# Optimization experiments

Hardware: AMD Instinct MI355X
Metric: run time of the kernel (lower is better)

The kernel has to match this reference:

```python
import jax, jax.numpy as jnp
import numpy as np

NB, B, T, D, H = 7, 16, 512, 128, 2
HD = D // H

def _ln(x, s, b):
    m = jnp.mean(x, -1, keepdims=True)
    v = jnp.mean((x - m) ** 2, -1, keepdims=True)
    return (x - m) * jax.lax.rsqrt(v + 1e-5) * s + b

def setup_inputs():
    key = jax.random.key(0)
    keys = iter(jax.random.split(key, 80))
    def w(*shape):
        return jax.random.normal(next(keys), shape, jnp.float32) * 0.02
    inp = {}
    inp['bands'] = jax.random.normal(next(keys), (NB, B, T, D), jnp.float32)
    for nm in ['Wq', 'Wk', 'Wv', 'Wo']:
        inp[nm] = w(NB, D, D)
    for nm in ['bq', 'bk', 'bv', 'bo']:
        inp[nm] = jnp.zeros((NB, D), jnp.float32)
    inp['g_ls'] = jnp.ones((3, D), jnp.float32); inp['g_lb'] = jnp.zeros((3, D), jnp.float32)
    inp['g_w1'] = w(3, D, 2 * D); inp['g_b1'] = jnp.zeros((3, 2 * D), jnp.float32)
    inp['g_w2'] = w(3, 2 * D, D); inp['g_b2'] = jnp.zeros((3, D), jnp.float32)
    inp['g_wg'] = w(3, D, D);     inp['g_bg'] = jnp.zeros((3, D), jnp.float32)
    inp['h_ls'] = jnp.ones((2, D), jnp.float32); inp['h_lb'] = jnp.zeros((2, D), jnp.float32)
    inp['h_w1'] = w(2, D, 3 * D); inp['h_b1'] = jnp.zeros((2, 3 * D), jnp.float32)
    inp['h_w2'] = w(2, 3 * D, D); inp['h_b2'] = jnp.zeros((2, D), jnp.float32)
    inp['r_ls'] = jnp.ones((2, D), jnp.float32); inp['r_lb'] = jnp.zeros((2, D), jnp.float32)
    inp['r_w1'] = w(2, D, 4 * D); inp['r_b1'] = jnp.zeros((2, 4 * D), jnp.float32)
    inp['r_w2'] = w(2, 4 * D, D); inp['r_b2'] = jnp.zeros((2, D), jnp.float32)
    # wormhole: pairs (0,6),(1,5),(2,4) share cross_proj per pair; bridge on band 3
    inp['wp_w'] = w(3, D, D);     inp['wp_b'] = jnp.zeros((3, D), jnp.float32)
    inp['wg_w'] = w(3, 2 * D, D); inp['wg_b'] = jnp.zeros((3, D), jnp.float32)
    inp['br_w'] = w(6, D, D);     inp['br_b'] = jnp.zeros((6, D), jnp.float32)
    inp['bg_w'] = w(2 * D, D);    inp['bg_b'] = jnp.zeros((D,), jnp.float32)
    return inp

def reference(bands, Wq, bq, Wk, bk, Wv, bv, Wo, bo,
              g_ls, g_lb, g_w1, g_b1, g_w2, g_b2, g_wg, g_bg,
              h_ls, h_lb, h_w1, h_b1, h_w2, h_b2,
              r_ls, r_lb, r_w1, r_b1, r_w2, r_b2,
              wp_w, wp_b, wg_w, wg_b, br_w, br_b, bg_w, bg_b):
    n, b, t, d = bands.shape
    # --- per-band causal self-attention, vectorized over the 7 bands ---
    def heads(x):  # [n,b,t,d] -> [n,b,H,t,hd]
        return x.reshape(n, b, t, H, HD).transpose(0, 1, 3, 2, 4)
    q = heads(jnp.einsum('nbtd,nde->nbte', bands, Wq) + bq[:, None, None, :])
    k = heads(jnp.einsum('nbtd,nde->nbte', bands, Wk) + bk[:, None, None, :])
    v = heads(jnp.einsum('nbtd,nde->nbte', bands, Wv) + bv[:, None, None, :])
    scores = jnp.einsum('nbhtd,nbhsd->nbhts', q, k) / np.float32(np.sqrt(HD))
    causal = jnp.triu(jnp.ones((t, t), bool), 1)
    scores = jnp.where(causal, jnp.float32(-1e9), scores)
    attn = jax.nn.softmax(scores, axis=-1)
    o = jnp.einsum('nbhts,nbhsd->nbhtd', attn, v)
    o = o.transpose(0, 1, 3, 2, 4).reshape(n, b, t, d)
    o = jnp.einsum('nbtd,nde->nbte', o, Wo) + bo[:, None, None, :]
    x = bands + o
    # --- band-tier FFN processors ---
    geo, hyb, rea = x[0:3], x[3:5], x[5:7]
    hg = _ln(geo, g_ls[:, None, None, :], g_lb[:, None, None, :])
    hg = jax.nn.gelu(jnp.einsum('nbtd,nde->nbte', hg, g_w1) + g_b1[:, None, None, :], approximate=False)
    hg = jnp.einsum('nbte,ned->nbtd', hg, g_w2) + g_b2[:, None, None, :]
    gate = jax.nn.sigmoid(jnp.einsum('nbtd,nde->nbte', geo, g_wg) + g_bg[:, None, None, :])
    geo = geo + gate * hg
    hh = _ln(hyb, h_ls[:, None, None, :], h_lb[:, None, None, :])
    hh = jax.nn.gelu(jnp.einsum('nbtd,nde->nbte', hh, h_w1) + h_b1[:, None, None, :], approximate=False)
    hyb = hyb + jnp.einsum('nbte,ned->nbtd', hh, h_w2) + h_b2[:, None, None, :]
    hr = _ln(rea, r_ls[:, None, None, :], r_lb[:, None, None, :])
    hr = jax.nn.gelu(jnp.einsum('nbtd,nde->nbte', hr, r_w1) + r_b1[:, None, None, :], approximate=False)
    rea = rea + jnp.einsum('nbte,ned->nbtd', hr, r_w2) + r_b2[:, None, None, :]
    y = jnp.concatenate([geo, hyb, rea], axis=0)
    # --- position-wise wormhole: pairs (0,6),(1,5),(2,4) + bridge band 3 ---
    bl = y[jnp.array([0, 1, 2])]   # low bands of each pair
    bh = y[jnp.array([6, 5, 4])]   # matching high bands
    info_lo = jnp.einsum('nbtd,nde->nbte', bh, wp_w) + wp_b[:, None, None, :]
    info_hi = jnp.einsum('nbtd,nde->nbte', bl, wp_w) + wp_b[:, None, None, :]
    gate_lo = jax.nn.sigmoid(jnp.einsum('nbtd,nde->nbte', jnp.concatenate([bl, info_lo], -1), wg_w) + wg_b[:, None, None, :])
    gate_hi = jax.nn.sigmoid(jnp.einsum('nbtd,nde->nbte', jnp.concatenate([bh, info_hi], -1), wg_w) + wg_b[:, None, None, :])
    out_lo = bl + gate_lo * info_lo
    out_hi = bh + gate_hi * info_hi
    others = y[jnp.array([0, 1, 2, 4, 5, 6])]
    bridge_info = (jnp.einsum('nbtd,nde->bte', others, br_w) + jnp.sum(br_b, 0)) / 6.0
    gate_br = jax.nn.sigmoid(jnp.concatenate([y[3], bridge_info], -1) @ bg_w + bg_b)
    out3 = y[3] + gate_br * bridge_info
    return jnp.stack([out_lo[0], out_lo[1], out_lo[2], out3, out_hi[2], out_hi[1], out_hi[0]], axis=0)
```

## Files before the change

### kernel.cpp

```cpp
#include <hip/hip_runtime.h>
#include <hip/hip_bf16.h>

#define NBAND 7
#define BBATCH 16
#define TSEQ 512
#define DMODEL 128
#define MBAND (BBATCH * TSEQ)
#define BANDE ((size_t)MBAND * DMODEL)

typedef __attribute__((ext_vector_type(8))) short short8;
typedef __attribute__((ext_vector_type(4))) float f32x4;
typedef unsigned int u32;
typedef unsigned short u16;

__device__ __forceinline__ u16 f2bf(float x) {
  unsigned u = __float_as_uint(x);
  unsigned r = u + 0x7FFF + ((u >> 16) & 1);
  return (u16)(r >> 16);
}
__device__ __forceinline__ u32 pack2(float a, float b) {
  return (u32)f2bf(a) | ((u32)f2bf(b) << 16);
}
__device__ __forceinline__ float b2f(u16 h) {
  return __uint_as_float((u32)h << 16);
}

struct TSlice { const float* src; u16* dst; int K, N; };
struct TArgs { TSlice s[62]; };

__global__ __launch_bounds__(256) void wtrans_kernel(TArgs a) {
  TSlice sl = a.s[blockIdx.z];
  const int tk = (blockIdx.x & 7) * 64, tn = (blockIdx.x >> 3) * 64;
  if (tk >= sl.K || tn >= sl.N) return;
  __shared__ __align__(16) u16 T[64][72];
  const int tid = threadIdx.x;
  #pragma unroll
  for (int it = 0; it < 4; ++it) {
    int idx = tid + it * 256;
    int k = idx >> 4, nq = (idx & 15) << 2;
    float4 v = *(const float4*)&sl.src[(size_t)(tk + k) * sl.N + tn + nq];
    T[nq + 0][k] = f2bf(v.x); T[nq + 1][k] = f2bf(v.y);
    T[nq + 2][k] = f2bf(v.z); T[nq + 3][k] = f2bf(v.w);
  }
  __syncthreads();
  #pragma unroll
  for (int it = 0; it < 2; ++it) {
    int idx = tid + it * 256;
    int n = idx >> 3, kq = (idx & 7) << 3;
    *(short8*)&sl.dst[(size_t)(tn + n) * sl.K + tk + kq] = *(const short8*)&T[n][kq];
  }
}

__device__ __forceinline__ void mfma_part_h(const u16* __restrict__ A,
                                            const u16* __restrict__ WT,
                                            int K, int m0, int n0, int tid,
                                            u16 (*As)[40], u16 (*Bs)[40],
                                            f32x4 acc[2][2]) {
  const int lane = tid & 63;
  const int wv = tid >> 6;
  const int wr = wv >> 1, wc = wv & 1;
  const int lr = lane & 15, k8 = lane >> 4;
  const int row = tid >> 2, kq = (tid & 3) << 3;

  for (int k0 = 0; k0 < K; k0 += 32) {
    *(short8*)&As[row][kq] = *(const short8*)&A[(size_t)(m0 + row) * K + k0 + kq];
    *(short8*)&Bs[row][kq] = *(const short8*)&WT[(size_t)(n0 + row) * K + k0 + kq];
    __syncthreads();
    short8 a0 = *(const short8*)&As[wr * 32 + lr][k8 * 8];
    short8 a1 = *(const short8*)&As[wr * 32 + 16 + lr][k8 * 8];
    short8 b0 = *(const short8*)&Bs[wc * 32 + lr][k8 * 8];
    short8 b1 = *(const short8*)&Bs[wc * 32 + 16 + lr][k8 * 8];
    acc[0][0] = __builtin_amdgcn_mfma_f32_16x16x32_bf16(a0, b0, acc[0][0], 0, 0, 0);
    acc[0][1] = __builtin_amdgcn_mfma_f32_16x16x32_bf16(a0, b1, acc[0][1], 0, 0, 0);
    acc[1][0] = __builtin_amdgcn_mfma_f32_16x16x32_bf16(a1, b0, acc[1][0], 0, 0, 0);
    acc[1][1] = __builtin_amdgcn_mfma_f32_16x16x32_bf16(a1, b1, acc[1][1], 0, 0, 0);
    __syncthreads();
  }
}

struct ZD {
  const u16 *A, *A2, *WT, *WT2;
  const float* bias;
  const float* residF;
  const u16 *residH, *extraH;
  float* OF;
  u16* OH;
  int K, N, op;
  int pad;
};
struct PArgs { ZD z[21]; };

__global__ __launch_bounds__(256) void gemm_b(PArgs p) {
  const ZD d = p.z[blockIdx.z];
  const int n0 = blockIdx.y * 64;
  if (n0 >= d.N) return;
  __shared__ __align__(16) u16 As[64][40];
  __shared__ __align__(16) u16 Bs[64][40];
  const int m0 = blockIdx.x * 64;
  const int tid = threadIdx.x;
  f32x4 acc[2][2] = {};

  mfma_part_h(d.A, d.WT, d.K, m0, n0, tid, As, Bs, acc);
  if (d.A2)
    mfma_part_h(d.A2, d.WT2, d.K, m0, n0, tid, As, Bs, acc);

  const int lane = tid & 63;
  const int wv = tid >> 6;
  const int wr = wv >> 1, wc = wv & 1;
  const int lr = lane & 15, lg = lane >> 4;

  #pragma unroll
  for (int i = 0; i < 2; ++i) {
    #pragma unroll
    for (int j = 0; j < 2; ++j) {
      #pragma unroll
      for (int r = 0; r < 4; ++r) {
        int m = m0 + wr * 32 + i * 16 + lg * 4 + r;
        int n = n0 + wc * 32 + j * 16 + lr;
        float v = acc[i][j][r];
        if (d.bias) v += d.bias[n];
        size_t idx = (size_t)m * d.N + n;
        switch (d.op) {
          case 0: d.OH[idx] = f2bf(v); break;
          case 1: d.OH[idx] =
                    f2bf(0.5f * v * (1.f + erff(v * 0.70710678118654752f))); break;
          case 2: d.OH[idx] = f2bf(1.f / (1.f + __expf(-v))); break;
          case 3: d.OH[idx] = f2bf(d.residF[idx] + v); break;
          case 4: {
            float gate = 1.f / (1.f + __expf(-v));
            d.OF[idx] = b2f(d.residH[idx]) + gate * b2f(d.extraH[idx]);
          } break;
          case 5: {
            float gm = d.extraH ? b2f(d.extraH[idx]) : 1.f;
            d.OH[idx] = f2bf(b2f(d.residH[idx]) + gm * v);
          } break;
        }
      }
    }
  }
}

__global__ __launch_bounds__(256) void bridge_kernel(const u16* __restrict__ yb,
                                                     const u16* __restrict__ wtBr,
                                                     const float* __restrict__ br_b,
                                                     u16* __restrict__ O) {
  __shared__ __align__(16) u16 As[64][40];
  __shared__ __align__(16) u16 Bs[64][40];
  const int m0 = blockIdx.x * 64, n0 = blockIdx.y * 64;
  const int tid = threadIdx.x;
  f32x4 acc[2][2] = {};
  const int bl[6] = {0, 1, 2, 4, 5, 6};
  for (int s = 0; s < 6; ++s)
    mfma_part_h(yb + (size_t)bl[s] * BANDE, wtBr + (size_t)s * 16384,
                128, m0, n0, tid, As, Bs, acc);

  const int lane = tid & 63;
  const int wv = tid >> 6;
  const int wr = wv >> 1, wc = wv & 1;
  const int lr = lane & 15, lg = lane >> 4;
  #pragma unroll
  for (int i = 0; i < 2; ++i)
    #pragma unroll
    for (int j = 0; j < 2; ++j) {
      int n = n0 + wc * 32 + j * 16 + lr;
      float bb = 0.f;
      #pragma unroll
      for (int s = 0; s < 6; ++s) bb += br_b[s * 128 + n];
      bb *= (1.f / 6.f);
      #pragma unroll
      for (int r = 0; r < 4; ++r) {
        int m = m0 + wr * 32 + i * 16 + lg * 4 + r;
        O[(size_t)m * 128 + n] = f2bf(acc[i][j][r] * (1.f / 6.f) + bb);
      }
    }
}

__global__ __launch_bounds__(256) void attn_kernel(const u16* __restrict__ q,
                                                   const u16* __restrict__ k,
                                                   const u16* __restrict__ v,
                                                   u16* __restrict__ o) {
  const int band = blockIdx.x >> 8;
  const int rest = blockIdx.x & 255;
  const int qt = 7 - (rest & 7);
  const int bh = rest >> 3;
  const int h  = bh & 1;
  const int b  = bh >> 1;
  const size_t rowbase = ((size_t)band * BBATCH + b) * TSEQ;

  const int tid  = threadIdx.x;
  const int w    = tid >> 6;
  const int lane = tid & 63;
  const int lr   = lane & 15;
  const int lg   = lane >> 4;

  __shared__ __align__(16) u16 Qs[64][72];
  __shared__ __align__(16) u16 Ks[64][72];
  __shared__ __align__(16) u16 Vs[64][72];
  __shared__ __align__(16) u16 Ps[4][16][72];

  #pragma unroll
  for (int it = 0; it < 2; ++it) {
    int idx = tid + it * 256;
    int r = idx >> 3, c8 = (idx & 7) << 3;
    *(short8*)&Qs[r][c8] =
        *(const short8*)&q[(rowbase + qt * 64 + r) * DMODEL + h * 64 + c8];
  }

  short8 kpre[2];
  u32 vpre[2][4];
  #pragma unroll
  for (int it = 0; it < 2; ++it) {
    int idx = tid + it * 256;
    int r = idx >> 3, c8 = (idx & 7) << 3;
    kpre[it] = *(const short8*)&k[(rowbase + r) * DMODEL + h * 64 + c8];
  }
  #pragma unroll
  for (int it = 0; it < 2; ++it) {
    int idx = tid + it * 256;
    int kp = idx >> 4, d0 = (idx & 15) << 2;
    size_t g0 = (rowbase + 2 * kp) * DMODEL + h * 64 + d0;
    vpre[it][0] = *(const u32*)&v[g0];
    vpre[it][1] = *(const u32*)&v[g0 + 2];
    vpre[it][2] = *(const u32*)&v[g0 + DMODEL];
    vpre[it][3] = *(const u32*)&v[g0 + DMODEL + 2];
  }

  f32x4 oacc[4] = {};
  float m[4], l[4];
  #pragma unroll
  for (int r = 0; r < 4; ++r) { m[r] = -1e30f; l[r] = 0.f; }

  for (int kt = 0; kt <= qt; ++kt) {
    __syncthreads();
    #pragma unroll
    for (int it = 0; it < 2; ++it) {
      int idx = tid + it * 256;
      int r = idx >> 3, c8 = (idx & 7) << 3;
      *(short8*)&Ks[r][c8] = kpre[it];
    }
    #pragma unroll
    for (int it = 0; it < 2; ++it) {
      int idx = tid + it * 256;
      int kp = idx >> 4, d0 = (idx & 15) << 2;
      u32 a0 = vpre[it][0], a1 = vpre[it][1];
      u32 b0 = vpre[it][2], b1 = vpre[it][3];
      *(u32*)&Vs[d0 + 0][2 * kp] = (a0 & 0xFFFFu) | (b0 << 16);
      *(u32*)&Vs[d0 + 1][2 * kp] = (a0 >> 16) | (b0 & 0xFFFF0000u);
      *(u32*)&Vs[d0 + 2][2 * kp] = (a1 & 0xFFFFu) | (b1 << 16);
      *(u32*)&Vs[d0 + 3][2 * kp] = (a1 >> 16) | (b1 & 0xFFFF0000u);
    }
    if (kt < qt) {
      int nt = kt + 1;
      #pragma unroll
      for (int it = 0; it < 2; ++it) {
        int idx = tid + it * 256;
        int r = idx >> 3, c8 = (idx & 7) << 3;
        kpre[it] = *(const short8*)&k[(rowbase + nt * 64 + r) * DMODEL + h * 64 + c8];
      }
      #pragma unroll
      for (int it = 0; it < 2; ++it) {
        int idx = tid + it * 256;
        int kp = idx >> 4, d0 = (idx & 15) << 2;
        size_t g0 = (rowbase + nt * 64 + 2 * kp) * DMODEL + h * 64 + d0;
        vpre[it][0] = *(const u32*)&v[g0];
        vpre[it][1] = *(const u32*)&v[g0 + 2];
        vpre[it][2] = *(const u32*)&v[g0 + DMODEL];
        vpre[it][3] = *(const u32*)&v[g0 + DMODEL + 2];
      }
    }
    __syncthreads();

    f32x4 s[4] = {};
    #pragma unroll
    for (int c = 0; c < 2; ++c) {
      short8 a = *(const short8*)&Qs[w * 16 + lr][c * 32 + lg * 8];
      #pragma unroll
      for (int j = 0; j < 4; ++j) {
        short8 bb = *(const short8*)&Ks[j * 16 + lr][c * 32 + lg * 8];
        s[j] = __builtin_amdgcn_mfma_f32_16x16x32_bf16(a, bb, s[j], 0, 0, 0);
      }
    }
    #pragma unroll
    for (int j = 0; j < 4; ++j)
      #pragma unroll
      for (int r = 0; r < 4; ++r)
        s[j][r] *= 0.125f;

    if (kt == qt) {
      #pragma unroll
      for (int j = 0; j < 4; ++j)
        #pragma unroll
        for (int r = 0; r < 4; ++r) {
          int row = w * 16 + lg * 4 + r;
          int col = j * 16 + lr;
          if (col > row) s[j][r] = -1e30f;
        }
    }

    float mx[4], al[4];
    #pragma unroll
    for (int r = 0; r < 4; ++r)
      mx[r] = fmaxf(fmaxf(s[0][r], s[1][r]), fmaxf(s[2][r], s[3][r]));
    #pragma unroll
    for (int off = 1; off <= 8; off <<= 1)
      #pragma unroll
      for (int r = 0; r < 4; ++r)
        mx[r] = fmaxf(mx[r], __shfl_xor(mx[r], off));
    #pragma unroll
    for (int r = 0; r < 4; ++r) {
      float mn = fmaxf(m[r], mx[r]);
      al[r] = __expf(m[r] - mn);
      m[r] = mn;
    }
    float rs[4] = {0.f, 0.f, 0.f, 0.f};
    #pragma unroll
    for (int j = 0; j < 4; ++j)
      #pragma unroll
      for (int r = 0; r < 4; ++r) {
        float pe = __expf(s[j][r] - m[r]);
        s[j][r] = pe;
        rs[r] += pe;
      }
    #pragma unroll
    for (int off = 1; off <= 8; off <<= 1)
      #pragma unroll
      for (int r = 0; r < 4; ++r)
        rs[r] += __shfl_xor(rs[r], off);
    #pragma unroll
    for (int r = 0; r < 4; ++r) l[r] = l[r] * al[r] + rs[r];

    #pragma unroll
    for (int j = 0; j < 4; ++j)
      #pragma unroll
      for (int r = 0; r < 4; ++r)
        oacc[j][r] *= al[r];

    #pragma unroll
    for (int j = 0; j < 4; ++j)
      #pragma unroll
      for (int r = 0; r < 4; ++r)
        Ps[w][lg * 4 + r][j * 16 + lr] = f2bf(s[j][r]);

    #pragma unroll
    for (int c = 0; c < 2; ++c) {
      short8 a = *(const short8*)&Ps[w][lr][c * 32 + lg * 8];
      #pragma unroll
      for (int j = 0; j < 4; ++j) {
        short8 bb = *(const short8*)&Vs[j * 16 + lr][c * 32 + lg * 8];
        oacc[j] = __builtin_amdgcn_mfma_f32_16x16x32_bf16(a, bb, oacc[j], 0, 0, 0);
      }
    }
  }

  float inv[4];
  #pragma unroll
  for (int r = 0; r < 4; ++r) inv[r] = 1.f / l[r];
  #pragma unroll
  for (int j = 0; j < 4; ++j)
    #pragma unroll
    for (int r = 0; r < 4; ++r) {
      size_t row = rowbase + qt * 64 + w * 16 + lg * 4 + r;
      o[row * DMODEL + h * 64 + j * 16 + lr] = f2bf(oacc[j][r] * inv[r]);
    }
}

struct LNA {
  const u16* x;
  u16* xn;
  const float* ls[7];
  const float* lb[7];
};

__global__ __launch_bounds__(256) void ln_kernel(LNA p) {
  const int tid = threadIdx.x;
  const int rr = tid >> 6, lane = tid & 63;
  const size_t row = (size_t)blockIdx.x * 4 + rr;
  u32 wv = *(const u32*)&p.x[row * DMODEL + 2 * lane];
  float a = b2f((u16)wv), b = b2f((u16)(wv >> 16));
  float s = a + b;
  #pragma unroll
  for (int off = 32; off; off >>= 1) s += __shfl_xor(s, off);
  float mean = s * (1.f / 128.f);
  float da = a - mean, db = b - mean;
  float vs = da * da + db * db;
  #pragma unroll
  for (int off = 32; off; off >>= 1) vs += __shfl_xor(vs, off);
  float rstd = rsqrtf(vs * (1.f / 128.f) + 1e-5f);
  int band = (int)(row >> 13);
  const float* ls = p.ls[band];
  const float* lb = p.lb[band];
  *(u32*)&p.xn[row * DMODEL + 2 * lane] =
      pack2(da * rstd * ls[2 * lane] + lb[2 * lane],
            db * rstd * ls[2 * lane + 1] + lb[2 * lane + 1]);
}

__global__ __launch_bounds__(256) void cvt_kernel(const float* __restrict__ in,
                                                  u16* __restrict__ out) {
  size_t i = ((size_t)blockIdx.x * 256 + threadIdx.x) * 8;
  float4 a = *(const float4*)&in[i];
  float4 b = *(const float4*)&in[i + 4];
  uint4 st = {pack2(a.x, a.y), pack2(a.z, a.w), pack2(b.x, b.y), pack2(b.z, b.w)};
  *(uint4*)&out[i] = st;
}

extern "C" void kernel_launch(void* const* d_in, const int* in_sizes, int n_in,
                              void* d_out, int out_size, void* d_ws, size_t ws_size,
                              hipStream_t stream) {
  bool dict = (in_sizes[2] != 896);
  const float* bands = (const float*)d_in[0];
  const float* Wq = (const float*)d_in[1];
  const float *Wk, *Wv, *Wo, *bq, *bk, *bv, *bo;
  if (dict) {
    Wk = (const float*)d_in[2]; Wv = (const float*)d_in[3]; Wo = (const float*)d_in[4];
    bq = (const float*)d_in[5]; bk = (const float*)d_in[6];
    bv = (const float*)d_in[7]; bo = (const float*)d_in[8];
  } else {
    bq = (const float*)d_in[2]; Wk = (const float*)d_in[3]; bk = (const float*)d_in[4];
    Wv = (const float*)d_in[5]; bv = (const float*)d_in[6];
    Wo = (const float*)d_in[7]; bo = (const float*)d_in[8];
  }
  const float* g_ls = (const float*)d_in[9];
  const float* g_lb = (const float*)d_in[10];
  const float* g_w1 = (const float*)d_in[11];
  const float* g_b1 = (const float*)d_in[12];
  const float* g_w2 = (const float*)d_in[13];
  const float* g_b2 = (const float*)d_in[14];
  const float* g_wg = (const float*)d_in[15];
  const float* g_bg = (const float*)d_in[16];
  const float* h_ls = (const float*)d_in[17];
  const float* h_lb = (const float*)d_in[18];
  const float* h_w1 = (const float*)d_in[19];
  const float* h_b1 = (const float*)d_in[20];
  const float* h_w2 = (const float*)d_in[21];
  const float* h_b2 = (const float*)d_in[22];
  const float* r_ls = (const float*)d_in[23];
  const float* r_lb = (const float*)d_in[24];
  const float* r_w1 = (const float*)d_in[25];
  const float* r_b1 = (const float*)d_in[26];
  const float* r_w2 = (const float*)d_in[27];
  const float* r_b2 = (const float*)d_in[28];
  const float* wp_w = (const float*)d_in[29];
  const float* wp_b = (const float*)d_in[30];
  const float* wg_w = (const float*)d_in[31];
  const float* wg_b = (const float*)d_in[32];
  const float* br_w = (const float*)d_in[33];
  const float* br_b = (const float*)d_in[34];
  const float* bg_w = (const float*)d_in[35];
  const float* bg_b = (const float*)d_in[36];
  float* out = (float*)d_out;

  const float* lsP[7] = {g_ls, g_ls + 128, g_ls + 256, h_ls, h_ls + 128, r_ls, r_ls + 128};
  const float* lbP[7] = {g_lb, g_lb + 128, g_lb + 256, h_lb, h_lb + 128, r_lb, r_lb + 128};
  const float* b1p[7] = {g_b1, g_b1 + 256, g_b1 + 512,
                         h_b1, h_b1 + 384, r_b1, r_b1 + 512};
  const float* b2p[7] = {g_b2, g_b2 + 128, g_b2 + 256,
                         h_b2, h_b2 + 128, r_b2, r_b2 + 128};
  const int hN[7] = {256, 256, 256, 384, 384, 512, 512};

  const size_t HIDSZ = (size_t)MBAND * 2560;
  u16* H = (u16*)d_ws;
  u16* hidh   = H;
  u16* bandsH = hidh;
  u16* qh = H + HIDSZ;
  u16* kh = qh + 7 * BANDE;
  u16* vh = kh + 7 * BANDE;
  u16* oh = vh + 7 * BANDE;
  u16* wt = oh + 7 * BANDE;
  u16* wtQ   = wt;
  u16* wtK   = wtQ + 7 * 16384;
  u16* wtV   = wtK + 7 * 16384;
  u16* wtO   = wtV + 7 * 16384;
  u16* wtGwg = wtO + 7 * 16384;
  u16* wtWp  = wtGwg + 3 * 16384;
  u16* wtBr  = wtWp + 3 * 16384;
  u16* wtWg  = wtBr + 6 * 16384;
  u16* wtBg  = wtWg + 6 * 16384;
  u16* wtG1  = wtBg + 2 * 16384;
  u16* wtH1  = wtG1 + 3 * 32768;
  u16* wtR1  = wtH1 + 2 * 49152;
  u16* wtG2  = wtR1 + 2 * 65536;
  u16* wtH2  = wtG2 + 3 * 32768;
  u16* wtR2  = wtH2 + 2 * 49152;
  u16* xh = qh;
  u16* xnh = kh;
  u16* gateh = vh;
  u16* yh = oh;
  u16* infoh = hidh;
  u16* bridgeh = hidh + 6 * BANDE;

  size_t hOff[7];
  {
    size_t acc = 0;
    for (int n = 0; n < 7; ++n) { hOff[n] = acc; acc += (size_t)MBAND * hN[n]; }
  }
  u16* wtW1s[7] = {wtG1, wtG1 + 32768, wtG1 + 65536,
                   wtH1, wtH1 + 49152, wtR1, wtR1 + 65536};
  u16* wtW2s[7] = {wtG2, wtG2 + 32768, wtG2 + 65536,
                   wtH2, wtH2 + 49152, wtR2, wtR2 + 65536};

  auto LP = [&](PArgs& p, int Z, int ymax) {
    dim3 grid(MBAND / 64, ymax, Z);
    gemm_b<<<grid, dim3(256), 0, stream>>>(p);
  };

  cvt_kernel<<<dim3((unsigned)(7 * BANDE / (8 * 256))), dim3(256), 0, stream>>>(bands, bandsH);

  {
    TArgs ta{};
    int ns = 0;
    auto add = [&](const float* s, u16* d, int K, int N) {
      ta.s[ns].src = s; ta.s[ns].dst = d; ta.s[ns].K = K; ta.s[ns].N = N; ++ns;
    };
    for (int z = 0; z < 7; ++z) add(Wq + z * 16384, wtQ + z * 16384, 128, 128);
    for (int z = 0; z < 7; ++z) add(Wk + z * 16384, wtK + z * 16384, 128, 128);
    for (int z = 0; z < 7; ++z) add(Wv + z * 16384, wtV + z * 16384, 128, 128);
    for (int z = 0; z < 7; ++z) add(Wo + z * 16384, wtO + z * 16384, 128, 128);
    for (int i = 0; i < 3; ++i) add(g_wg + i * 16384, wtGwg + i * 16384, 128, 128);
    for (int i = 0; i < 3; ++i) add(wp_w + i * 16384, wtWp + i * 16384, 128, 128);
    for (int j = 0; j < 6; ++j) add(br_w + j * 16384, wtBr + j * 16384, 128, 128);
    for (int i = 0; i < 3; ++i) {
      add(wg_w + i * 32768,         wtWg + (size_t)(2 * i) * 16384,     128, 128);
      add(wg_w + i * 32768 + 16384, wtWg + (size_t)(2 * i + 1) * 16384, 128, 128);
    }
    add(bg_w,         wtBg,         128, 128);
    add(bg_w + 16384, wtBg + 16384, 128, 128);
    for (int i = 0; i < 3; ++i) add(g_w1 + i * 32768, wtG1 + i * 32768, 128, 256);
    for (int i = 0; i < 2; ++i) add(h_w1 + i * 49152, wtH1 + i * 49152, 128, 384);
    for (int i = 0; i < 2; ++i) add(r_w1 + i * 65536, wtR1 + i * 65536, 128, 512);
    for (int i = 0; i < 3; ++i) add(g_w2 + i * 32768, wtG2 + i * 32768, 256, 128);
    for (int i = 0; i < 2; ++i) add(h_w2 + i * 49152, wtH2 + i * 49152, 384, 128);
    for (int i = 0; i < 2; ++i) add(r_w2 + i * 65536, wtR2 + i * 65536, 512, 128);
    wtrans_kernel<<<dim3(64, 1, 62), dim3(256), 0, stream>>>(ta);
  }

  {
    PArgs p{};
    const u16* wtQKV[3] = {wtQ, wtK, wtV};
    const float* bqkv[3] = {bq, bk, bv};
    u16* oqkv[3] = {qh, kh, vh};
    for (int w = 0; w < 3; ++w)
      for (int band = 0; band < 7; ++band) {
        ZD& d = p.z[w * 7 + band];
        d.A = bandsH + (size_t)band * BANDE;
        d.WT = wtQKV[w] + (size_t)band * 16384;
        d.bias = bqkv[w] + band * 128;
        d.OH = oqkv[w] + (size_t)band * BANDE;
        d.K = 128; d.N = 128; d.op = 0;
      }
    LP(p, 21, 2);
  }

  attn_kernel<<<dim3(NBAND * 256), dim3(256), 0, stream>>>(qh, kh, vh, oh);

  {
    PArgs p{};
    for (int band = 0; band < 7; ++band) {
      ZD& d = p.z[band];
      d.A = oh + (size_t)band * BANDE;
      d.WT = wtO + (size_t)band * 16384;
      d.bias = bo + band * 128;
      d.residF = bands + (size_t)band * BANDE;
      d.OH = xh + (size_t)band * BANDE;
      d.K = 128; d.N = 128; d.op = 3;
    }
    LP(p, 7, 2);
  }

  {
    LNA p{};
    p.x = xh; p.xn = xnh;
    for (int n = 0; n < 7; ++n) { p.ls[n] = lsP[n]; p.lb[n] = lbP[n]; }
    ln_kernel<<<dim3(NBAND * MBAND / 4), dim3(256), 0, stream>>>(p);
  }

  {
    PArgs p{};
    for (int z = 0; z < 3; ++z) {
      ZD& d = p.z[z];
      d.A = xh + (size_t)z * BANDE;
      d.WT = wtGwg + (size_t)z * 16384;
      d.bias = g_bg + z * 128;
      d.OH = gateh + (size_t)z * BANDE;
      d.K = 128; d.N = 128; d.op = 2;
    }
    for (int band = 0; band < 7; ++band) {
      ZD& d = p.z[3 + band];
      d.A = xnh + (size_t)band * BANDE;
      d.WT = wtW1s[band];
      d.bias = b1p[band];
      d.OH = hidh + hOff[band];
      d.K = 128; d.N = hN[band]; d.op = 1;
    }
    LP(p, 10, 8);
  }

  {
    PArgs p{};
    for (int band = 0; band < 7; ++band) {
      ZD& d = p.z[band];
      d.A = hidh + hOff[band];
      d.WT = wtW2s[band];
      d.bias = b2p[band];
      d.residH = xh + (size_t)band * BANDE;
      d.extraH = (band < 3) ? gateh + (size_t)band * BANDE : nullptr;
      d.OH = yh + (size_t)band * BANDE;
      d.K = hN[band]; d.N = 128; d.op = 5;
    }
    LP(p, 7, 2);
  }

  {
    PArgs p{};
    for (int z = 0; z < 6; ++z) {
      int t = (z < 3) ? z : z + 1;
      int src = 6 - t;
      int i = (t < 3) ? t : 6 - t;
      ZD& d = p.z[z];
      d.A = yh + (size_t)src * BANDE;
      d.WT = wtWp + (size_t)i * 16384;
      d.bias = wp_b + i * 128;
      d.OH = infoh + (size_t)z * BANDE;
      d.K = 128; d.N = 128; d.op = 0;
    }
    LP(p, 6, 2);
  }

  bridge_kernel<<<dim3(MBAND / 64, 2), dim3(256), 0, stream>>>(yh, wtBr, br_b, bridgeh);

  {
    PArgs p{};
    for (int z = 0; z < 6; ++z) {
      int t = (z < 3) ? z : z + 1;
      int i = (t < 3) ? t : 6 - t;
      ZD& d = p.z[z];
      d.A = yh + (size_t)t * BANDE;
      d.WT = wtWg + (size_t)(2 * i) * 16384;
      d.A2 = infoh + (size_t)z * BANDE;
      d.WT2 = wtWg + (size_t)(2 * i + 1) * 16384;
      d.bias = wg_b + i * 128;
      d.residH = yh + (size_t)t * BANDE;
      d.extraH = infoh + (size_t)z * BANDE;
      d.OF = out + (size_t)t * BANDE;
      d.K = 128; d.N = 128; d.op = 4;
    }
    {
      ZD& d = p.z[6];
      d.A = yh + 3 * BANDE;
      d.WT = wtBg;
      d.A2 = bridgeh;
      d.WT2 = wtBg + 16384;
      d.bias = bg_b;
      d.residH = yh + 3 * BANDE;
      d.extraH = bridgeh;
      d.OF = out + 3 * BANDE;
      d.K = 128; d.N = 128; d.op = 4;
    }
    LP(p, 7, 2);
  }
}
```

Before: 239.1 us.

## Write V transposed from projection GEMM and keep Q fragments in registers

After: 239.0 us. About the same (-0.0%).

```diff
diff --git a/kernel.cpp b/kernel.cpp
--- a/kernel.cpp
+++ b/kernel.cpp
@@ -134,6 +134,7 @@
             float gm = d.extraH ? b2f(d.extraH[idx]) : 1.f;
             d.OH[idx] = f2bf(b2f(d.residH[idx]) + gm * v);
           } break;
+          case 6: d.OH[(size_t)n * MBAND + m] = f2bf(v); break;
         }
       }
     }
@@ -177,7 +178,7 @@
 
 __global__ __launch_bounds__(256) void attn_kernel(const u16* __restrict__ q,
                                                    const u16* __restrict__ k,
-                                                   const u16* __restrict__ v,
+                                                   const u16* __restrict__ vT,
                                                    u16* __restrict__ o) {
   const int band = blockIdx.x >> 8;
   const int rest = blockIdx.x & 255;
@@ -186,6 +187,7 @@
   const int h  = bh & 1;
   const int b  = bh >> 1;
   const size_t rowbase = ((size_t)band * BBATCH + b) * TSEQ;
+  const u16* vb = vT + (size_t)band * BANDE + (size_t)h * 64 * MBAND + (size_t)b * TSEQ;
 
   const int tid  = threadIdx.x;
   const int w    = tid >> 6;
@@ -193,36 +195,24 @@
   const int lr   = lane & 15;
   const int lg   = lane >> 4;
 
-  __shared__ __align__(16) u16 Qs[64][72];
   __shared__ __align__(16) u16 Ks[64][72];
   __shared__ __align__(16) u16 Vs[64][72];
   __shared__ __align__(16) u16 Ps[4][16][72];
 
-  #pragma unroll
-  for (int it = 0; it < 2; ++it) {
-    int idx = tid + it * 256;
-    int r = idx >> 3, c8 = (idx & 7) << 3;
-    *(short8*)&Qs[r][c8] =
-        *(const short8*)&q[(rowbase + qt * 64 + r) * DMODEL + h * 64 + c8];
-  }
-
-  short8 kpre[2];
-  u32 vpre[2][4];
+  short8 aq[2];
+  {
+    const u16* qp = &q[(rowbase + qt * 64 + w * 16 + lr) * DMODEL + h * 64 + lg * 8];
+    aq[0] = *(const short8*)qp;
+    aq[1] = *(const short8*)(qp + 32);
+  }
+
+  short8 kpre[2], vpre[2];
   #pragma unroll
   for (int it = 0; it < 2; ++it) {
     int idx = tid + it * 256;
     int r = idx >> 3, c8 = (idx & 7) << 3;
     kpre[it] = *(const short8*)&k[(rowbase + r) * DMODEL + h * 64 + c8];
-  }
-  #pragma unroll
-  for (int it = 0; it < 2; ++it) {
-    int idx = tid + it * 256;
-    int kp = idx >> 4, d0 = (idx & 15) << 2;
-    size_t g0 = (rowbase + 2 * kp) * DMODEL + h * 64 + d0;
-    vpre[it][0] = *(const u32*)&v[g0];
-    vpre[it][1] = *(const u32*)&v[g0 + 2];
-    vpre[it][2] = *(const u32*)&v[g0 + DMODEL];
-    vpre[it][3] = *(const u32*)&v[g0 + DMODEL + 2];
+    vpre[it] = *(const short8*)&vb[(size_t)r * MBAND + c8];
   }
 
   f32x4 oacc[4] = {};
@@ -237,17 +227,7 @@
       int idx = tid + it * 256;
       int r = idx >> 3, c8 = (idx & 7) << 3;
       *(short8*)&Ks[r][c8] = kpre[it];
-    }
-    #pragma unroll
-    for (int it = 0; it < 2; ++it) {
-      int idx = tid + it * 256;
-      int kp = idx >> 4, d0 = (idx & 15) << 2;
-      u32 a0 = vpre[it][0], a1 = vpre[it][1];
-      u32 b0 = vpre[it][2], b1 = vpre[it][3];
-      *(u32*)&Vs[d0 + 0][2 * kp] = (a0 & 0xFFFFu) | (b0 << 16);
-      *(u32*)&Vs[d0 + 1][2 * kp] = (a0 >> 16) | (b0 & 0xFFFF0000u);
-      *(u32*)&Vs[d0 + 2][2 * kp] = (a1 & 0xFFFFu) | (b1 << 16);
-      *(u32*)&Vs[d0 + 3][2 * kp] = (a1 >> 16) | (b1 & 0xFFFF0000u);
+      *(short8*)&Vs[r][c8] = vpre[it];
     }
     if (kt < qt) {
       int nt = kt + 1;
@@ -256,24 +236,15 @@
         int idx = tid + it * 256;
         int r = idx >> 3, c8 = (idx & 7) << 3;
         kpre[it] = *(const short8*)&k[(rowbase + nt * 64 + r) * DMODEL + h * 64 + c8];
+        vpre[it] = *(const short8*)&vb[(size_t)r * MBAND + nt * 64 + c8];
       }
-      #pragma unroll
-      for (int it = 0; it < 2; ++it) {
-        int idx = tid + it * 256;
-        int kp = idx >> 4, d0 = (idx & 15) << 2;
-        size_t g0 = (rowbase + nt * 64 + 2 * kp) * DMODEL + h * 64 + d0;
-        vpre[it][0] = *(const u32*)&v[g0];
-        vpre[it][1] = *(const u32*)&v[g0 + 2];
-        vpre[it][2] = *(const u32*)&v[g0 + DMODEL];
-        vpre[it][3] = *(const u32*)&v[g0 + DMODEL + 2];
-      }
     }
     __syncthreads();
 
     f32x4 s[4] = {};
     #pragma unroll
     for (int c = 0; c < 2; ++c) {
-      short8 a = *(const short8*)&Qs[w * 16 + lr][c * 32 + lg * 8];
+      short8 a = aq[c];
       #pragma unroll
       for (int j = 0; j < 4; ++j) {
         short8 bb = *(const short8*)&Ks[j * 16 + lr][c * 32 + lg * 8];
@@ -545,7 +516,7 @@
         d.WT = wtQKV[w] + (size_t)band * 16384;
         d.bias = bqkv[w] + band * 128;
         d.OH = oqkv[w] + (size_t)band * BANDE;
-        d.K = 128; d.N = 128; d.op = 0;
+        d.K = 128; d.N = 128; d.op = (w == 2) ? 6 : 0;
       }
     LP(p, 21, 2);
   }
```
